# Optimization experiments

Measured on AMD Instinct MI355X. Metric: run time of the kernel, lower is better.

Reference implementation:

```python
import jax, jax.numpy as jnp
import numpy as np
from jax.scipy.special import logsumexp

L = 15      # DATA_MAX_SEG_LEN
K = 64      # XCRIBE_DIM
H = 16      # SEG_DIM
TAG = 32    # TAG_DIM
DUR = 4     # DURATION_DIM
NY = 15     # len(LABELS)
N = 16384   # sequence length
S = 2048    # number of gold segments
NEG = jnp.float32(-1e30)


def setup_inputs() -> dict:
    key = jax.random.key(0)
    ks = jax.random.split(key, 24)
    sL = 1.0 / np.sqrt(H)
    sV = 1.0 / np.sqrt(2 * H + TAG + DUR)
    sW = 1.0 / np.sqrt(H)

    def U(k, shape, s):
        return jax.random.uniform(k, shape, jnp.float32, -s, s)

    return dict(
        data=jax.random.normal(ks[0], (N, K), jnp.float32),
        fwd_Wih=U(ks[1], (4 * H, K), sL), fwd_Whh=U(ks[2], (4 * H, H), sL),
        fwd_bih=U(ks[3], (4 * H,), sL), fwd_bhh=U(ks[4], (4 * H,), sL),
        bwd_Wih=U(ks[5], (4 * H, K), sL), bwd_Whh=U(ks[6], (4 * H, H), sL),
        bwd_bih=U(ks[7], (4 * H,), sL), bwd_bhh=U(ks[8], (4 * H,), sL),
        fwd_h0=jax.random.normal(ks[9], (H,), jnp.float32),
        fwd_c0=jax.random.normal(ks[10], (H,), jnp.float32),
        bwd_h0=jax.random.normal(ks[11], (H,), jnp.float32),
        bwd_c0=jax.random.normal(ks[12], (H,), jnp.float32),
        Y_enc=jax.random.normal(ks[13], (NY, TAG), jnp.float32),
        Z_enc=jax.random.normal(ks[14], (L, DUR), jnp.float32),
        V_W=U(ks[15], (H, 2 * H + TAG + DUR), sV), V_b=U(ks[16], (H,), sV),
        W_W=U(ks[17], (1, H), sW), W_b=U(ks[18], (1,), sW),
        tags=jax.random.randint(ks[19], (S,), 0, NY),
        lengths=jax.random.randint(ks[20], (S,), 1, L + 1),
    )


def _lstm(xs, Wih, Whh, bih, bhh, h0, c0):
    # xs: [L, B, K] -> hidden outputs [L, B, H]; torch gate order i,f,g,o
    B = xs.shape[1]
    b = bih + bhh

    def step(carry, x):
        h, c = carry
        g = x @ Wih.T + h @ Whh.T + b
        i, f, gg, o = jnp.split(g, 4, axis=-1)
        c = jax.nn.sigmoid(f) * c + jax.nn.sigmoid(i) * jnp.tanh(gg)
        h = jax.nn.sigmoid(o) * jnp.tanh(c)
        return (h, c), h

    init = (jnp.broadcast_to(h0, (B, H)), jnp.broadcast_to(c0, (B, H)))
    _, hs = jax.lax.scan(step, init, xs)
    return hs


def reference(data, fwd_Wih, fwd_Whh, fwd_bih, fwd_bhh, fwd_h0, fwd_c0,
              bwd_Wih, bwd_Whh, bwd_bih, bwd_bhh, bwd_h0, bwd_c0,
              Y_enc, Z_enc, V_W, V_b, W_W, W_b, tags, lengths):
    n = data.shape[0]
    pos = jnp.arange(n)[:, None]      # [N,1]
    dd = jnp.arange(L)[None, :]       # [1,L]
    idx_f = jnp.minimum(pos + dd, n - 1)   # forward window indices
    idx_b = pos - dd                       # backward window indices (may be <0)

    win_f = data[idx_f].transpose(1, 0, 2)                  # [L,N,K]
    win_b = data[jnp.maximum(idx_b, 0)].transpose(1, 0, 2)  # [L,N,K]

    # fwd[i,d] = forward_precalc[i][i+d]; bwd[e,d] = backward_precalc[e-d][e]
    fwd = _lstm(win_f, fwd_Wih, fwd_Whh, fwd_bih, fwd_bhh, fwd_h0, fwd_c0).transpose(1, 0, 2)
    bwd = _lstm(win_b, bwd_Wih, bwd_Whh, bwd_bih, bwd_bhh, bwd_h0, bwd_c0).transpose(1, 0, 2)

    # gather fwd at (start=e-d, duration index d) -> aligned with end position e
    fwd_g = fwd[jnp.maximum(idx_b, 0), dd]          # [N,L,H]
    fb = jnp.concatenate([fwd_g, bwd], axis=-1)     # [N,L,2H]

    # split V across concat blocks: [fwd,bwd | Y | Z]
    V1 = V_W[:, :2 * H]; V2 = V_W[:, 2 * H:2 * H + TAG]; V3 = V_W[:, 2 * H + TAG:]
    base = fb @ V1.T + (Z_enc @ V3.T)[None, :, :] + V_b      # [N,L,H]
    ypart = Y_enc @ V2.T                                     # [NY,H]
    pre = base[:, :, None, :] + ypart[None, None, :, :]      # [N,L,NY,H]
    scores = jnp.tanh(pre) @ W_W[0] + W_b[0]                 # [N,L,NY]

    valid = idx_b >= 0
    A = jnp.where(valid, logsumexp(scores, axis=-1), NEG)    # [N,L] lse over labels

    # semi-Markov forward DP: log_alpha[i] = lse_d(log_alpha[i-d] + A[i-1,d-1])
    def dp(hist, a):  # hist[k] = log_alpha[i-1-k]
        new = logsumexp(hist + a)
        return jnp.concatenate([new[None], hist[:-1]]), new

    hist0 = jnp.full((L,), NEG, jnp.float32).at[0].set(0.0)
    _, alphas = jax.lax.scan(dp, hist0, A)
    logZ = alphas[-1]

    # gold-segment score; original never advances `chars`, so start is always 0
    gv = lengths < L
    gscores = scores[lengths - 1, lengths - 1, tags]
    indiv = jnp.sum(jnp.where(gv, gscores, 0.0))
    return logZ - indiv
```

## Files before the change

### kernel.cpp

```cpp
#include <hip/hip_runtime.h>

#define NPOS 16384
#define NEG  (-1e30f)

#define OFF_FWDH  0
#define OFF_BWDH  1966080
#define OFF_A     3932160
#define OFF_T0    4194304
#define OFF_R     4251904
#define OFF_GSC   4255504
#define OFF_CTR   4255744

struct Params {
    const float *data, *fWih, *fWhh, *fbih, *fbhh, *bWih, *bWhh, *bbih, *bbhh;
    const float *h0f, *c0f, *h0b, *c0b, *Yenc, *Zenc, *VW, *Vb, *WW, *Wb;
    const int *tags, *lengths;
    float *ws; float *out;
};

typedef _Float16 half2_t __attribute__((ext_vector_type(2)));

__device__ __forceinline__ half2_t u2h(unsigned int v) {
    return __builtin_bit_cast(half2_t, v);
}
__device__ __forceinline__ unsigned int packh(float a, float b) {
    half2_t h = { (_Float16)a, (_Float16)b };
    return __builtin_bit_cast(unsigned int, h);
}
__device__ __forceinline__ float fdot2_(unsigned int w, unsigned int x, float acc) {
    return __builtin_amdgcn_fdot2(u2h(w), u2h(x), acc, false);
}
__device__ __forceinline__ float sigf(float x) {
    return __builtin_amdgcn_rcpf(1.0f + __expf(-x));
}
__device__ __forceinline__ float tanhf_(float x) {
    return 1.0f - 2.0f * __builtin_amdgcn_rcpf(1.0f + __expf(2.0f * x));
}
__device__ __forceinline__ float lse15(const float* tv) {
    float a0 = fmaxf(tv[0], tv[1]),  a1 = fmaxf(tv[2], tv[3]);
    float a2 = fmaxf(tv[4], tv[5]),  a3 = fmaxf(tv[6], tv[7]);
    float a4 = fmaxf(tv[8], tv[9]),  a5 = fmaxf(tv[10], tv[11]);
    float a6 = fmaxf(tv[12], tv[13]);
    float b0 = fmaxf(a0, a1), b1 = fmaxf(a2, a3), b2 = fmaxf(a4, a5), b3 = fmaxf(a6, tv[14]);
    float mx = fmaxf(fmaxf(b0, b1), fmaxf(b2, b3));
    float e[15];
    #pragma unroll
    for (int i = 0; i < 15; i++) e[i] = __expf(tv[i] - mx);
    float s0 = e[0]+e[1], s1 = e[2]+e[3], s2 = e[4]+e[5], s3 = e[6]+e[7];
    float s4 = e[8]+e[9], s5 = e[10]+e[11], s6 = e[12]+e[13];
    float t0 = s0+s1, t1 = s2+s3, t2 = s4+s5, t3 = s6+e[14];
    return mx + __logf((t0+t1) + (t2+t3));
}

__global__ __launch_bounds__(512) void kA(Params p)
{
    __shared__ unsigned int xs2[78*33];
    __shared__ float xgT[64*78];
    __shared__ unsigned int hsh[2*512];
    __shared__ unsigned int wqx[2048];
    __shared__ unsigned int wqh[512];
    __shared__ float bq[64];

    const int tid  = threadIdx.x;
    const int lane = tid & 63;
    const int wq   = __builtin_amdgcn_readfirstlane(tid >> 6);
    const int dir  = blockIdx.y;
    const int P0   = blockIdx.x << 6;
    const int dbase = P0 - (dir ? 14 : 0);

    if (blockIdx.x == 0 && dir == 0 && tid == 0)
        ((unsigned int*)(p.ws + OFF_CTR))[0] = 0;

    const float* Wih = dir ? p.bWih : p.fWih;
    const float* Whh = dir ? p.bWhh : p.fWhh;
    const float* bih = dir ? p.bbih : p.fbih;
    const float* bhh = dir ? p.bbhh : p.fbhh;
    const float* h0  = dir ? p.h0b  : p.h0f;
    const float* c0  = dir ? p.c0b  : p.c0f;

    for (int e = tid; e < 2048; e += 512) {
        int k2 = e >> 6, pi = e & 63;
        int w = pi >> 3, jj = pi & 7;
        int j = ((jj >> 1) << 4) + 2*w + (jj & 1);
        wqx[e] = packh(Wih[j*64 + 2*k2], Wih[j*64 + 2*k2 + 1]);
    }
    if (tid < 512) {
        int m2 = tid >> 6, pi = tid & 63;
        int w = pi >> 3, jj = pi & 7;
        int j = ((jj >> 1) << 4) + 2*w + (jj & 1);
        wqh[tid] = packh(Whh[j*16 + 2*m2], Whh[j*16 + 2*m2 + 1]);
    }
    if (tid < 64) {
        int w = tid >> 3, jj = tid & 7;
        int j = ((jj >> 1) << 4) + 2*w + (jj & 1);
        bq[tid] = bih[j] + bhh[j];
    }
    for (int idx = tid; idx < 78*32; idx += 512) {
        int r = idx >> 5, c = idx & 31;
        int q = dbase + r;
        q = q < 0 ? 0 : (q > NPOS-1 ? NPOS-1 : q);
        float2 x2 = *(const float2*)(p.data + (size_t)q*64 + c*2);
        xs2[r*33 + c] = packh(x2.x, x2.y);
    }
    if (tid < 512) {
        int m2 = tid >> 6;
        hsh[tid] = packh(h0[2*m2], h0[2*m2 + 1]);
    }
    __syncthreads();

    #pragma unroll
    for (int pass = 0; pass < 2; pass++) {
        int r = pass*64 + lane;
        if (r < 78) {
            float acc[8];
            #pragma unroll
            for (int jj = 0; jj < 8; jj++) acc[jj] = bq[wq*8 + jj];
            #pragma unroll 8
            for (int k2 = 0; k2 < 32; k2++) {
                unsigned int xp = xs2[r*33 + k2];
                uint4 w0 = *(const uint4*)&wqx[k2*64 + wq*8];
                uint4 w1 = *(const uint4*)&wqx[k2*64 + wq*8 + 4];
                acc[0] = fdot2_(w0.x, xp, acc[0]);
                acc[1] = fdot2_(w0.y, xp, acc[1]);
                acc[2] = fdot2_(w0.z, xp, acc[2]);
                acc[3] = fdot2_(w0.w, xp, acc[3]);
                acc[4] = fdot2_(w1.x, xp, acc[4]);
                acc[5] = fdot2_(w1.y, xp, acc[5]);
                acc[6] = fdot2_(w1.z, xp, acc[6]);
                acc[7] = fdot2_(w1.w, xp, acc[7]);
            }
            #pragma unroll
            for (int jj = 0; jj < 8; jj++) xgT[(wq*8 + jj)*78 + r] = acc[jj];
        }
    }
    float cv0 = c0[wq*2], cv1 = c0[wq*2 + 1];
    unsigned int* outH = (unsigned int*)(p.ws + (dir ? OFF_BWDH : OFF_FWDH));
    __syncthreads();

    int buf = 0;
    for (int d = 0; d < 15; d++) {
        const int row = dir ? (lane + 14 - d) : (lane + d);
        float part[8];
        #pragma unroll
        for (int jj = 0; jj < 8; jj++) part[jj] = xgT[(wq*8 + jj)*78 + row];
        #pragma unroll
        for (int m2 = 0; m2 < 8; m2++) {
            unsigned int hp = hsh[buf*512 + m2*64 + lane];
            uint4 w0 = *(const uint4*)&wqh[m2*64 + wq*8];
            uint4 w1 = *(const uint4*)&wqh[m2*64 + wq*8 + 4];
            part[0] = fdot2_(w0.x, hp, part[0]);
            part[1] = fdot2_(w0.y, hp, part[1]);
            part[2] = fdot2_(w0.z, hp, part[2]);
            part[3] = fdot2_(w0.w, hp, part[3]);
            part[4] = fdot2_(w1.x, hp, part[4]);
            part[5] = fdot2_(w1.y, hp, part[5]);
            part[6] = fdot2_(w1.z, hp, part[6]);
            part[7] = fdot2_(w1.w, hp, part[7]);
        }
        float cn0 = sigf(part[2])*cv0 + sigf(part[0])*tanhf_(part[4]);
        float cn1 = sigf(part[3])*cv1 + sigf(part[1])*tanhf_(part[5]);
        cv0 = cn0; cv1 = cn1;
        float h0v = sigf(part[6])*tanhf_(cn0);
        float h1v = sigf(part[7])*tanhf_(cn1);
        unsigned int pk = packh(h0v, h1v);
        hsh[(buf^1)*512 + wq*64 + lane] = pk;
        outH[((size_t)d*NPOS + P0 + lane)*8 + wq] = pk;
        __syncthreads();
        buf ^= 1;
    }
}

__global__ __launch_bounds__(1024) void kBC(Params p)
{
    __shared__ float As[64*17];
    __shared__ unsigned int VWh[256];
    __shared__ float zbl[240];
    __shared__ float EY[240];
    const int tid = threadIdx.x;
    const int P0  = blockIdx.x << 6;
    float* ws = p.ws;

    if (tid < 240) {
        int y = tid >> 4, h = tid & 15;
        float acc = 0.f;
        for (int t = 0; t < 32; t++) acc += p.Yenc[y*32 + t] * p.VW[h*68 + 32 + t];
        EY[tid] = __expf(acc + acc);
        float z = p.Vb[h];
        for (int u = 0; u < 4; u++) z += p.Zenc[y*4 + u] * p.VW[h*68 + 64 + u];
        zbl[tid] = z;
    }
    if (tid < 256) {
        int h = tid >> 4, j2 = tid & 15;
        int col = (j2 < 8) ? 2*j2 : 16 + 2*(j2 - 8);
        VWh[tid] = packh(p.VW[h*68 + col], p.VW[h*68 + col + 1]);
    }
    __syncthreads();

    const int pl = tid & 63;
    const int d  = tid >> 6;
    const int pp = P0 + pl;
    float Aval = NEG;
    if (d < 15 && pp >= d) {
        const uint4* fptr = (const uint4*)((const unsigned int*)(ws + OFF_FWDH)
                            + ((size_t)d*NPOS + (pp - d))*8);
        const uint4* bptr = (const uint4*)((const unsigned int*)(ws + OFF_BWDH)
                            + ((size_t)d*NPOS + pp)*8);
        uint4 f0 = fptr[0], f1 = fptr[1];
        uint4 b0 = bptr[0], b1 = bptr[1];
        unsigned int fp_[8] = {f0.x, f0.y, f0.z, f0.w, f1.x, f1.y, f1.z, f1.w};
        unsigned int bp_[8] = {b0.x, b0.y, b0.z, b0.w, b1.x, b1.y, b1.z, b1.w};
        float E[16], w2[16], wsum = 0.f;
        #pragma unroll
        for (int h = 0; h < 16; h++) {
            float acc = zbl[d*16 + h];
            uint4 va = *(const uint4*)&VWh[h*16];
            uint4 vb = *(const uint4*)&VWh[h*16 + 4];
            uint4 vc = *(const uint4*)&VWh[h*16 + 8];
            uint4 vd = *(const uint4*)&VWh[h*16 + 12];
            acc = fdot2_(va.x, fp_[0], acc); acc = fdot2_(va.y, fp_[1], acc);
            acc = fdot2_(va.z, fp_[2], acc); acc = fdot2_(va.w, fp_[3], acc);
            acc = fdot2_(vb.x, fp_[4], acc); acc = fdot2_(vb.y, fp_[5], acc);
            acc = fdot2_(vb.z, fp_[6], acc); acc = fdot2_(vb.w, fp_[7], acc);
            acc = fdot2_(vc.x, bp_[0], acc); acc = fdot2_(vc.y, bp_[1], acc);
            acc = fdot2_(vc.z, bp_[2], acc); acc = fdot2_(vc.w, bp_[3], acc);
            acc = fdot2_(vd.x, bp_[4], acc); acc = fdot2_(vd.y, bp_[5], acc);
            acc = fdot2_(vd.z, bp_[6], acc); acc = fdot2_(vd.w, bp_[7], acc);
            E[h] = __expf(acc + acc);
            float w = p.WW[h];
            w2[h] = -2.0f * w;
            wsum += w;
        }
        const float cst = p.Wb[0] + wsum;
        float sc[15];
        #pragma unroll
        for (int y = 0; y < 15; y++) {
            float a = 0.f;
            #pragma unroll
            for (int h = 0; h < 16; h++)
                a = fmaf(w2[h], __builtin_amdgcn_rcpf(1.0f + E[h]*EY[y*16 + h]), a);
            sc[y] = cst + a;
        }
        Aval = lse15(sc);
        if (pp == d && pp < 15) {
            float* gsc = ws + OFF_GSC;
            #pragma unroll
            for (int y = 0; y < 15; y++) gsc[pp*15 + y] = sc[y];
        }
    }
    As[pl*17 + d] = Aval;
    __syncthreads();

    if (tid < 15) {
        const int j = tid;
        float s[15];
        #pragma unroll
        for (int i = 0; i < 15; i++) s[i] = (i == j) ? 0.f : NEG;
        #pragma unroll 4
        for (int t = 0; t < 64; t++) {
            float tv[15];
            #pragma unroll
            for (int i = 0; i < 15; i++) tv[i] = s[i] + As[t*17 + i];
            float nw = lse15(tv);
            #pragma unroll
            for (int i = 14; i > 0; i--) s[i] = s[i-1];
            s[0] = nw;
        }
        float* T0 = ws + OFF_T0;
        #pragma unroll
        for (int i = 0; i < 15; i++) T0[blockIdx.x*225 + i*15 + j] = s[i];
    }
}

__global__ __launch_bounds__(256) void kDE(Params p)
{
    __shared__ float sm[4084];
    __shared__ int lastFlag;
    const int tid = threadIdx.x;
    const int b   = blockIdx.x;
    unsigned int* ctr = (unsigned int*)(p.ws + OFF_CTR);

    {
        float* Rm = sm;
        const float* T0 = p.ws + OFF_T0;
        const int e = tid, i2 = e / 15, j2 = e % 15;
        const int c0 = b * 16;
        if (e < 225) Rm[i2*16 + j2] = T0[c0*225 + e];
        __syncthreads();
        for (int t = 1; t < 16; t++) {
            float nw = 0.f;
            if (e < 225) {
                const float* Trow = T0 + (c0 + t)*225 + i2*15;
                float tv[15];
                #pragma unroll
                for (int k = 0; k < 15; k++) tv[k] = Trow[k] + Rm[k*16 + j2];
                nw = lse15(tv);
            }
            __syncthreads();
            if (e < 225) Rm[i2*16 + j2] = nw;
            __syncthreads();
        }
        if (e < 225) p.ws[OFF_R + b*225 + e] = Rm[i2*16 + j2];
    }
    __syncthreads();
    __threadfence();
    if (tid == 0) {
        unsigned int old = __hip_atomic_fetch_add(&ctr[0], 1u, __ATOMIC_ACQ_REL,
                                                  __HIP_MEMORY_SCOPE_AGENT);
        lastFlag = (old == 15u);
    }
    __syncthreads();
    if (!lastFlag) return;
    __threadfence();

    {
        float* RA  = sm;
        float* G   = sm + 3840;
        float* red = sm + 4080;
        const float* Rg = p.ws + OFF_R;
        for (int idx = tid; idx < 16*225; idx += 256) {
            int t = idx / 225, r = idx % 225;
            RA[t*240 + (r/15)*16 + (r%15)] = Rg[idx];
        }
        __syncthreads();
        const int e = tid, i2 = e / 15, j2 = e % 15;
        if (e < 225) G[i2*16 + j2] = RA[i2*16 + j2];
        __syncthreads();
        for (int t = 1; t < 16; t++) {
            float nw = 0.f;
            if (e < 225) {
                float tv[15];
                #pragma unroll
                for (int k = 0; k < 15; k++) tv[k] = RA[t*240 + i2*16 + k] + G[k*16 + j2];
                nw = lse15(tv);
            }
            __syncthreads();
            if (e < 225) G[i2*16 + j2] = nw;
            __syncthreads();
        }
        const float* gsc = p.ws + OFF_GSC;
        float loc = 0.f;
        for (int s = tid; s < 2048; s += 256) {
            int len = p.lengths[s];
            if (len < 15) loc += gsc[(len-1)*15 + p.tags[s]];
        }
        #pragma unroll
        for (int off = 32; off > 0; off >>= 1) loc += __shfl_down(loc, off);
        if ((tid & 63) == 0) red[tid >> 6] = loc;
        __syncthreads();
        if (tid == 0) {
            float ind = red[0] + red[1] + red[2] + red[3];
            p.out[0] = G[0] - ind;
        }
    }
}

extern "C" void kernel_launch(void* const* d_in, const int* in_sizes, int n_in,
                              void* d_out, int out_size, void* d_ws, size_t ws_size,
                              hipStream_t stream)
{
    Params prm;
    prm.data = (const float*)d_in[0];
    prm.fWih = (const float*)d_in[1];
    prm.fWhh = (const float*)d_in[2];
    prm.fbih = (const float*)d_in[3];
    prm.fbhh = (const float*)d_in[4];
    prm.bWih = (const float*)d_in[5];
    prm.bWhh = (const float*)d_in[6];
    prm.bbih = (const float*)d_in[7];
    prm.bbhh = (const float*)d_in[8];
    prm.h0f  = (const float*)d_in[9];
    prm.c0f  = (const float*)d_in[10];
    prm.h0b  = (const float*)d_in[11];
    prm.c0b  = (const float*)d_in[12];
    prm.Yenc = (const float*)d_in[13];
    prm.Zenc = (const float*)d_in[14];
    prm.VW   = (const float*)d_in[15];
    prm.Vb   = (const float*)d_in[16];
    prm.WW   = (const float*)d_in[17];
    prm.Wb   = (const float*)d_in[18];
    prm.tags    = (const int*)d_in[19];
    prm.lengths = (const int*)d_in[20];
    prm.ws  = (float*)d_ws;
    prm.out = (float*)d_out;

    hipLaunchKernelGGL(kA,  dim3(256, 2), dim3(512),  0, stream, prm);
    hipLaunchKernelGGL(kBC, dim3(256),    dim3(1024), 0, stream, prm);
    hipLaunchKernelGGL(kDE, dim3(16),     dim3(256),  0, stream, prm);
}
```

Baseline: 191.6 us.

## Parallelize semi-Markov DP chain with tree reduction of log-semiring matrix products

```diff
diff --git a/kernel.cpp b/kernel.cpp
--- a/kernel.cpp
+++ b/kernel.cpp
@@ -50,6 +50,24 @@
     float s4 = e[8]+e[9], s5 = e[10]+e[11], s6 = e[12]+e[13];
     float t0 = s0+s1, t1 = s2+s3, t2 = s4+s5, t3 = s6+e[14];
     return mx + __logf((t0+t1) + (t2+t3));
+}
+
+__device__ __forceinline__ void lse_mm(const float* src, float* dst, int nprod,
+                                       int tid, int nthr)
+{
+    const int tot = nprod * 225;
+    for (int e = tid; e < tot; e += nthr) {
+        const int m = e / 225;
+        const int r = e - m * 225;
+        const int i = r / 15;
+        const int j = r - i * 15;
+        const float* Ar = src + (2*m + 1)*240 + i*16;
+        const float* Bc = src + (2*m)*240 + j;
+        float tv[15];
+        #pragma unroll
+        for (int k = 0; k < 15; k++) tv[k] = Ar[k] + Bc[k*16];
+        dst[m*240 + i*16 + j] = lse15(tv);
+    }
 }
 
 __global__ __launch_bounds__(512) void kA(Params p)
@@ -176,6 +194,8 @@
     __shared__ unsigned int VWh[256];
     __shared__ float zbl[240];
     __shared__ float EY[240];
+    __shared__ float Ms[16*240];
+    __shared__ float Mp[8*240];
     const int tid = threadIdx.x;
     const int P0  = blockIdx.x << 6;
     float* ws = p.ws;
@@ -250,56 +270,71 @@
     As[pl*17 + d] = Aval;
     __syncthreads();
 
-    if (tid < 15) {
-        const int j = tid;
-        float s[15];
-        #pragma unroll
-        for (int i = 0; i < 15; i++) s[i] = (i == j) ? 0.f : NEG;
-        #pragma unroll 4
-        for (int t = 0; t < 64; t++) {
-            float tv[15];
-            #pragma unroll
-            for (int i = 0; i < 15; i++) tv[i] = s[i] + As[t*17 + i];
-            float nw = lse15(tv);
-            #pragma unroll
-            for (int i = 14; i > 0; i--) s[i] = s[i-1];
-            s[0] = nw;
-        }
-        float* T0 = ws + OFF_T0;
-        #pragma unroll
-        for (int i = 0; i < 15; i++) T0[blockIdx.x*225 + i*15 + j] = s[i];
-    }
-}
-
-__global__ __launch_bounds__(256) void kDE(Params p)
+    {
+        const int wv = tid >> 6;
+        const int ln = tid & 63;
+        if (ln < 15) {
+            float s[15];
+            #pragma unroll
+            for (int i = 0; i < 15; i++) s[i] = (i == ln) ? 0.f : NEG;
+            const int t0 = wv * 4;
+            #pragma unroll
+            for (int q = 0; q < 4; q++) {
+                const int t = t0 + q;
+                float tv[15];
+                #pragma unroll
+                for (int i = 0; i < 15; i++) tv[i] = s[i] + As[t*17 + i];
+                float nw = lse15(tv);
+                #pragma unroll
+                for (int i = 14; i > 0; i--) s[i] = s[i-1];
+                s[0] = nw;
+            }
+            #pragma unroll
+            for (int i = 0; i < 15; i++) Ms[wv*240 + i*16 + ln] = s[i];
+        }
+    }
+    __syncthreads();
+
+    lse_mm(Ms, Mp, 8, tid, 1024);  __syncthreads();
+    lse_mm(Mp, Ms, 4, tid, 1024);  __syncthreads();
+    lse_mm(Ms, Mp, 2, tid, 1024);  __syncthreads();
+    if (tid < 225) {
+        const int i = tid / 15, j = tid - (tid / 15) * 15;
+        float tv[15];
+        #pragma unroll
+        for (int k = 0; k < 15; k++) tv[k] = Mp[240 + i*16 + k] + Mp[k*16 + j];
+        (ws + OFF_T0)[blockIdx.x*225 + i*15 + j] = lse15(tv);
+    }
+}
+
+__global__ __launch_bounds__(1024) void kDE(Params p)
 {
-    __shared__ float sm[4084];
+    __shared__ float RA[16*240];
+    __shared__ float RP[8*240];
+    __shared__ float red[16];
+    __shared__ float logZsh;
     __shared__ int lastFlag;
     const int tid = threadIdx.x;
     const int b   = blockIdx.x;
     unsigned int* ctr = (unsigned int*)(p.ws + OFF_CTR);
 
     {
-        float* Rm = sm;
         const float* T0 = p.ws + OFF_T0;
-        const int e = tid, i2 = e / 15, j2 = e % 15;
-        const int c0 = b * 16;
-        if (e < 225) Rm[i2*16 + j2] = T0[c0*225 + e];
+        for (int idx = tid; idx < 16*225; idx += 1024) {
+            int t = idx / 225, r = idx - t*225;
+            RA[t*240 + (r/15)*16 + (r%15)] = T0[(b*16 + t)*225 + r];
+        }
         __syncthreads();
-        for (int t = 1; t < 16; t++) {
-            float nw = 0.f;
-            if (e < 225) {
-                const float* Trow = T0 + (c0 + t)*225 + i2*15;
-                float tv[15];
-                #pragma unroll
-                for (int k = 0; k < 15; k++) tv[k] = Trow[k] + Rm[k*16 + j2];
-                nw = lse15(tv);
-            }
-            __syncthreads();
-            if (e < 225) Rm[i2*16 + j2] = nw;
-            __syncthreads();
-        }
-        if (e < 225) p.ws[OFF_R + b*225 + e] = Rm[i2*16 + j2];
+        lse_mm(RA, RP, 8, tid, 1024); __syncthreads();
+        lse_mm(RP, RA, 4, tid, 1024); __syncthreads();
+        lse_mm(RA, RP, 2, tid, 1024); __syncthreads();
+        if (tid < 225) {
+            const int i = tid / 15, j = tid - (tid / 15) * 15;
+            float tv[15];
+            #pragma unroll
+            for (int k = 0; k < 15; k++) tv[k] = RP[240 + i*16 + k] + RP[k*16 + j];
+            p.ws[OFF_R + b*225 + i*15 + j] = lse15(tv);
+        }
     }
     __syncthreads();
     __threadfence();
@@ -313,33 +348,24 @@
     __threadfence();
 
     {
-        float* RA  = sm;
-        float* G   = sm + 3840;
-        float* red = sm + 4080;
         const float* Rg = p.ws + OFF_R;
-        for (int idx = tid; idx < 16*225; idx += 256) {
-            int t = idx / 225, r = idx % 225;
-            RA[t*240 + (r/15)*16 + (r%15)] = Rg[idx];
+        for (int idx = tid; idx < 16*225; idx += 1024) {
+            int t = idx / 225, r = idx - t*225;
+            RA[t*240 + (r/15)*16 + (r%15)] = Rg[t*225 + r];
         }
         __syncthreads();
-        const int e = tid, i2 = e / 15, j2 = e % 15;
-        if (e < 225) G[i2*16 + j2] = RA[i2*16 + j2];
-        __syncthreads();
-        for (int t = 1; t < 16; t++) {
-            float nw = 0.f;
-            if (e < 225) {
-                float tv[15];
-                #pragma unroll
-                for (int k = 0; k < 15; k++) tv[k] = RA[t*240 + i2*16 + k] + G[k*16 + j2];
-                nw = lse15(tv);
-            }
-            __syncthreads();
-            if (e < 225) G[i2*16 + j2] = nw;
-            __syncthreads();
+        lse_mm(RA, RP, 8, tid, 1024); __syncthreads();
+        lse_mm(RP, RA, 4, tid, 1024); __syncthreads();
+        lse_mm(RA, RP, 2, tid, 1024); __syncthreads();
+        if (tid == 0) {
+            float tv[15];
+            #pragma unroll
+            for (int k = 0; k < 15; k++) tv[k] = RP[240 + k] + RP[k*16];
+            logZsh = lse15(tv);
         }
         const float* gsc = p.ws + OFF_GSC;
         float loc = 0.f;
-        for (int s = tid; s < 2048; s += 256) {
+        for (int s = tid; s < 2048; s += 1024) {
             int len = p.lengths[s];
             if (len < 15) loc += gsc[(len-1)*15 + p.tags[s]];
         }
@@ -348,8 +374,10 @@
         if ((tid & 63) == 0) red[tid >> 6] = loc;
         __syncthreads();
         if (tid == 0) {
-            float ind = red[0] + red[1] + red[2] + red[3];
-            p.out[0] = G[0] - ind;
+            float ind = 0.f;
+            #pragma unroll
+            for (int q = 0; q < 16; q++) ind += red[q];
+            p.out[0] = logZsh - ind;
         }
     }
 }
@@ -385,5 +413,5 @@
 
     hipLaunchKernelGGL(kA,  dim3(256, 2), dim3(512),  0, stream, prm);
     hipLaunchKernelGGL(kBC, dim3(256),    dim3(1024), 0, stream, prm);
-    hipLaunchKernelGGL(kDE, dim3(16),     dim3(256),  0, stream, prm);
-}
+    hipLaunchKernelGGL(kDE, dim3(16),     dim3(1024), 0, stream, prm);
+}
```

New measurement: 170.7 us. 1.12x faster.
